# Kernel tuning notes

Measured on AMD Instinct MI355X. Metric: run time of the kernel, lower is better.

Reference implementation:

```python
import jax, jax.numpy as jnp
import numpy as np

N_NODES = 50000
N_EDGES = 1600000
IN_C, HID_C, OUT_C = 256, 256, 10


def setup_inputs() -> dict:
    key = jax.random.key(0)
    ks = jax.random.split(key, 8)
    x = jax.random.normal(ks[0], (N_NODES, IN_C), dtype=jnp.float32)
    edge_index = jax.random.randint(ks[1], (2, N_EDGES), 0, N_NODES, dtype=jnp.int64)
    s1 = 1.0 / np.sqrt(IN_C)
    s2 = 1.0 / np.sqrt(HID_C)
    W1l = jax.random.normal(ks[2], (IN_C, HID_C), dtype=jnp.float32) * s1
    W1r = jax.random.normal(ks[3], (IN_C, HID_C), dtype=jnp.float32) * s1
    b1 = jnp.zeros((HID_C,), dtype=jnp.float32)
    W2l = jax.random.normal(ks[4], (HID_C, OUT_C), dtype=jnp.float32) * s2
    W2r = jax.random.normal(ks[5], (HID_C, OUT_C), dtype=jnp.float32) * s2
    b2 = jnp.zeros((OUT_C,), dtype=jnp.float32)
    return {"x": x, "edge_index": edge_index, "W1l": W1l, "W1r": W1r,
            "b1": b1, "W2l": W2l, "W2r": W2r, "b2": b2}


def _mean_agg(x, src, dst, n):
    # scatter-mean of source features into destination nodes
    summed = jax.ops.segment_sum(x[src], dst, num_segments=n)  # [N, C]
    cnt = jax.ops.segment_sum(jnp.ones_like(dst, dtype=x.dtype), dst, num_segments=n)
    return summed / jnp.maximum(cnt, 1.0)[:, None]


def _sage_conv(x, src, dst, Wl, Wr, b):
    # PyG SAGEConv (mean aggr): lin_l(mean_j x_j) + lin_r(x_i) + bias
    n = x.shape[0]
    agg = _mean_agg(x, src, dst, n)
    return agg @ Wl + x @ Wr + b


def reference(x, edge_index, W1l, W1r, b1, W2l, W2r, b2):
    src = edge_index[0]
    dst = edge_index[1]
    h = _sage_conv(x, src, dst, W1l, W1r, b1)
    h = jax.nn.relu(h)  # dropout skipped: eval mode
    out = _sage_conv(h, src, dst, W2l, W2r, b2)
    return jax.nn.log_softmax(out, axis=1)
```

## Files before the change

### kernel.cpp

```cpp
#include <hip/hip_runtime.h>
#include <hip/hip_bf16.h>

#define N_NODES 50000
#define N_EDGES 1600000
#define IN_C 256
#define HID_C 256
#define OUT_C 10
#define CD_STRIDE 32
#define SLOT_CAP 96
#define NBUCKET 196
#define EBUF_CAP 9216

typedef short bf16x8 __attribute__((ext_vector_type(8)));
typedef float f32x4 __attribute__((ext_vector_type(4)));

static __device__ __forceinline__ float b2f(short v) {
    unsigned u = (unsigned)(unsigned short)v << 16;
    return __builtin_bit_cast(float, u);
}
static __device__ __forceinline__ short f2b(float f) {
    __hip_bfloat16 h = __float2bfloat16(f);
    return __builtin_bit_cast(short, h);
}

__global__ __launch_bounds__(256) void k_part(const int* __restrict__ src,
                                              const int* __restrict__ dst,
                                              int* __restrict__ g_cursor,
                                              int* __restrict__ ebuf) {
    __shared__ int hist[NBUCKET];
    __shared__ int base[NBUCKET];
    __shared__ int pos[NBUCKET];
    int tid = threadIdx.x;
    if (tid < NBUCKET) { hist[tid] = 0; pos[tid] = 0; }
    __syncthreads();

    int4 s[4], d[4];
    bool valid[4];
#pragma unroll
    for (int q = 0; q < 4; ++q) {
        int idx = blockIdx.x * 1024 + q * 256 + tid;
        valid[q] = (idx < N_EDGES / 4);
        if (valid[q]) {
            s[q] = ((const int4*)src)[idx];
            d[q] = ((const int4*)dst)[idx];
        }
    }
#pragma unroll
    for (int q = 0; q < 4; ++q) {
        if (valid[q]) {
            atomicAdd(&hist[d[q].x >> 8], 1);
            atomicAdd(&hist[d[q].y >> 8], 1);
            atomicAdd(&hist[d[q].z >> 8], 1);
            atomicAdd(&hist[d[q].w >> 8], 1);
        }
    }
    __syncthreads();
    if (tid < NBUCKET && hist[tid] > 0)
        base[tid] = atomicAdd(&g_cursor[tid], hist[tid]);
    __syncthreads();
#pragma unroll
    for (int q = 0; q < 4; ++q) {
        if (valid[q]) {
            int ss[4] = { s[q].x, s[q].y, s[q].z, s[q].w };
            int dd[4] = { d[q].x, d[q].y, d[q].z, d[q].w };
#pragma unroll
            for (int e = 0; e < 4; ++e) {
                int b = dd[e] >> 8;
                int p = base[b] + atomicAdd(&pos[b], 1);
                if (p < EBUF_CAP)
                    ebuf[b * EBUF_CAP + p] = ss[e] | ((dd[e] & 255) << 16);
            }
        }
    }
}

__global__ __launch_bounds__(256) void k_bucket(const int* __restrict__ ebuf,
                                                const int* __restrict__ g_cursor,
                                                int* __restrict__ cnt,
                                                unsigned short* __restrict__ slots) {
    __shared__ int lcnt[256];
    int b = blockIdx.x, tid = threadIdx.x;
    lcnt[tid] = 0;
    __syncthreads();
    int n_e = g_cursor[b];
    if (n_e > EBUF_CAP) n_e = EBUF_CAP;
    const int* eb = ebuf + b * EBUF_CAP;
    int n4 = n_e >> 2;
    for (int t = tid; t < n4; t += 256) {
        int4 v = ((const int4*)eb)[t];
        int vv[4] = { v.x, v.y, v.z, v.w };
#pragma unroll
        for (int e = 0; e < 4; ++e) {
            int dl = (vv[e] >> 16) & 255;
            int sv = vv[e] & 0xFFFF;
            int p = atomicAdd(&lcnt[dl], 1);
            if (p < SLOT_CAP) slots[(size_t)(b * 256 + dl) * SLOT_CAP + p] = (unsigned short)sv;
        }
    }
    for (int t = (n4 << 2) + tid; t < n_e; t += 256) {
        int vv = eb[t];
        int dl = (vv >> 16) & 255;
        int sv = vv & 0xFFFF;
        int p = atomicAdd(&lcnt[dl], 1);
        if (p < SLOT_CAP) slots[(size_t)(b * 256 + dl) * SLOT_CAP + p] = (unsigned short)sv;
    }
    __syncthreads();
    int nid = b * 256 + tid;
    if (nid < N_NODES) cnt[nid] = lcnt[tid];
}

__global__ void k_cvt_x(const float4* __restrict__ x, short4* __restrict__ xb) {
    int i = blockIdx.x * 256 + threadIdx.x;
    float4 v = x[i];
    short4 o = { f2b(v.x), f2b(v.y), f2b(v.z), f2b(v.w) };
    xb[i] = o;
}

__global__ void k_prep_w(const float* __restrict__ W1l, const float* __restrict__ W1r,
                         __hip_bfloat16* __restrict__ Wt) {
    int idx = blockIdx.x * 256 + threadIdx.x;
    int n = idx >> 8, k = idx & 255;
    float v = (n < HID_C) ? W1l[k * HID_C + n] : W1r[k * HID_C + (n - HID_C)];
    Wt[idx] = __float2bfloat16(v);
}

__global__ void k_prep_w2f(const float* __restrict__ W2l, const float* __restrict__ W2r,
                           float* __restrict__ Wt2f) {
    int idx = blockIdx.x * 256 + threadIdx.x;
    int r = idx >> 8, k = idx & 255;
    if (r < OUT_C) Wt2f[r * 256 + k] = W2l[k * OUT_C + r];
    else           Wt2f[(16 + r - OUT_C) * 256 + k] = W2r[k * OUT_C + (r - OUT_C)];
}

__global__ __launch_bounds__(256) void k_gemm1(
        const __hip_bfloat16* __restrict__ Xb, const __hip_bfloat16* __restrict__ Wt,
        const float* __restrict__ b1,
        __hip_bfloat16* __restrict__ Ab, __hip_bfloat16* __restrict__ Bh) {
    __shared__ short Smem[2 * 128 * 64];
    short* As = Smem;
    short* Bs = Smem + 128 * 64;
    int tid = threadIdx.x;
    int wave = tid >> 6, lane = tid & 63;
    int r = lane & 15, quad = lane >> 4;
    int wr = wave >> 1, wc = wave & 1;
    int m_base = blockIdx.x * 128;
    int n_base = blockIdx.y * 128;

    int srow = tid >> 3;
    int kb8  = (tid & 7) * 16;
    int swz  = kb8 ^ ((srow & 7) << 4);

    f32x4 acc[4][4];
#pragma unroll
    for (int i = 0; i < 4; ++i)
#pragma unroll
        for (int j = 0; j < 4; ++j) acc[i][j] = f32x4{0.f, 0.f, 0.f, 0.f};

    int4 av[4], bv[4];
#pragma unroll
    for (int q = 0; q < 4; ++q) {
        int grow = m_base + q * 32 + srow;
        if (grow > N_NODES - 1) grow = N_NODES - 1;
        av[q] = *(const int4*)((const char*)Xb + ((size_t)grow * 512 + kb8));
        int brow = n_base + q * 32 + srow;
        bv[q] = *(const int4*)((const char*)Wt + ((size_t)brow * 512 + kb8));
    }

    for (int kk = 0; kk < 4; ++kk) {
        if (kk) __syncthreads();
#pragma unroll
        for (int q = 0; q < 4; ++q) {
            *(int4*)((char*)As + (size_t)((q * 32 + srow) * 128 + swz)) = av[q];
            *(int4*)((char*)Bs + (size_t)((q * 32 + srow) * 128 + swz)) = bv[q];
        }
        __syncthreads();

        if (kk < 3) {
            int kbyte = (kk + 1) * 128 + kb8;
#pragma unroll
            for (int q = 0; q < 4; ++q) {
                int grow = m_base + q * 32 + srow;
                if (grow > N_NODES - 1) grow = N_NODES - 1;
                av[q] = *(const int4*)((const char*)Xb + ((size_t)grow * 512 + kbyte));
                int brow = n_base + q * 32 + srow;
                bv[q] = *(const int4*)((const char*)Wt + ((size_t)brow * 512 + kbyte));
            }
        }

#pragma unroll
        for (int s = 0; s < 2; ++s) {
            int kfb = (s * 64 + quad * 16) ^ ((r & 7) << 4);
            bf16x8 a[4], b[4];
#pragma unroll
            for (int i = 0; i < 4; ++i)
                a[i] = *(const bf16x8*)((const char*)As + (size_t)((wr * 64 + i * 16 + r) * 128) + kfb);
#pragma unroll
            for (int j = 0; j < 4; ++j)
                b[j] = *(const bf16x8*)((const char*)Bs + (size_t)((wc * 64 + j * 16 + r) * 128) + kfb);
#pragma unroll
            for (int i = 0; i < 4; ++i)
#pragma unroll
                for (int j = 0; j < 4; ++j)
                    acc[i][j] = __builtin_amdgcn_mfma_f32_16x16x32_bf16(a[i], b[j], acc[i][j], 0, 0, 0);
        }
    }

    __syncthreads();
    short* Cs = Smem;
    bool left = (n_base < HID_C);
#pragma unroll
    for (int j = 0; j < 4; ++j) {
        int coll = wc * 64 + 16 * j + r;
        float bias = left ? 0.f : b1[n_base + coll - HID_C];
#pragma unroll
        for (int i = 0; i < 4; ++i) {
#pragma unroll
            for (int ii = 0; ii < 4; ++ii) {
                int rowl = wr * 64 + 16 * i + quad * 4 + ii;
                int byteoff = (coll * 2) ^ ((rowl & 7) << 4);
                *(short*)((char*)Cs + rowl * 256 + byteoff) = f2b(acc[i][j][ii] + bias);
            }
        }
    }
    __syncthreads();

    int rrow = tid >> 4;
    int cchunk = (tid & 15) * 16;
    size_t colbyte = left ? (size_t)(n_base * 2) : (size_t)((n_base - HID_C) * 2);
    char* outp = left ? (char*)Ab : (char*)Bh;
    for (int rb = 0; rb < 128; rb += 16) {
        int rowl = rb + rrow;
        int4 v = *(const int4*)((const char*)Cs + rowl * 256 + (cchunk ^ ((rowl & 7) << 4)));
        int grow = m_base + rowl;
        if (grow < N_NODES)
            *(int4*)(outp + (size_t)grow * 512 + colbyte + cchunk) = v;
    }
}

__global__ __launch_bounds__(256) void k_agg1f(
        const __hip_bfloat16* __restrict__ Ab, const __hip_bfloat16* __restrict__ Bh,
        const int* __restrict__ cnt, const unsigned short* __restrict__ slots,
        const float* __restrict__ Wt2f, const float* __restrict__ b2,
        float* __restrict__ CD) {
    int wave = threadIdx.x >> 6, lane = threadIdx.x & 63;
    int nid = blockIdx.x * 4 + wave;
    int half = lane >> 5;
    int c8 = (lane & 31) * 8;
    const unsigned short* row = slots + (size_t)nid * SLOT_CAP;
    int n = cnt[nid];
    if (n > SLOT_CAP) n = SLOT_CAP;
    int mid = (n + 1) >> 1;
    int beg = half ? mid : 0;
    int end = half ? n : mid;

    float s0[8], s1[8], s2[8], s3[8];
#pragma unroll
    for (int j = 0; j < 8; ++j) { s0[j] = 0.f; s1[j] = 0.f; s2[j] = 0.f; s3[j] = 0.f; }

    const __hip_bfloat16* abc = Ab + c8;
    int e = beg;
    for (; e + 4 <= end; e += 4) {
        int i0 = row[e], i1 = row[e + 1], i2 = row[e + 2], i3 = row[e + 3];
        bf16x8 v0 = *(const bf16x8*)(abc + (size_t)i0 * HID_C);
        bf16x8 v1 = *(const bf16x8*)(abc + (size_t)i1 * HID_C);
        bf16x8 v2 = *(const bf16x8*)(abc + (size_t)i2 * HID_C);
        bf16x8 v3 = *(const bf16x8*)(abc + (size_t)i3 * HID_C);
#pragma unroll
        for (int j = 0; j < 8; ++j) {
            s0[j] += b2f(v0[j]); s1[j] += b2f(v1[j]);
            s2[j] += b2f(v2[j]); s3[j] += b2f(v3[j]);
        }
    }
    for (; e < end; ++e) {
        int i0 = row[e];
        bf16x8 v0 = *(const bf16x8*)(abc + (size_t)i0 * HID_C);
#pragma unroll
        for (int j = 0; j < 8; ++j) s0[j] += b2f(v0[j]);
    }
#pragma unroll
    for (int j = 0; j < 8; ++j) s0[j] += (s1[j] + s2[j]) + s3[j];
#pragma unroll
    for (int j = 0; j < 8; ++j) s0[j] += __shfl_down(s0[j], 32, 64);

    float h[8];
    float inv = 1.f / fmaxf((float)n, 1.f);
    if (half == 0) {
        bf16x8 bb = *(const bf16x8*)(Bh + (size_t)nid * HID_C + c8);
#pragma unroll
        for (int j = 0; j < 8; ++j)
            h[j] = fmaxf(s0[j] * inv + b2f(bb[j]), 0.f);
    }
#pragma unroll
    for (int j = 0; j < 8; ++j) h[j] = __shfl(h[j], lane & 31, 64);

    const float* wbase = Wt2f + (half ? 16 * 256 : 0);
    float acc[10];
#pragma unroll
    for (int j = 0; j < 10; ++j) {
        f32x4 w0 = *(const f32x4*)(wbase + j * 256 + c8);
        f32x4 w1 = *(const f32x4*)(wbase + j * 256 + c8 + 4);
        float a = h[0] * w0[0] + h[1] * w0[1] + h[2] * w0[2] + h[3] * w0[3]
                + h[4] * w1[0] + h[5] * w1[1] + h[6] * w1[2] + h[7] * w1[3];
#pragma unroll
        for (int off = 16; off > 0; off >>= 1)
            a += __shfl_down(a, off, 32);
        acc[j] = a;
    }
    if ((lane & 31) == 0) {
        float* o = CD + (size_t)nid * CD_STRIDE + half * 16;
        if (half == 0) {
#pragma unroll
            for (int j = 0; j < 10; ++j) o[j] = acc[j];
            o[10] = 0.f; o[11] = 0.f;
        } else {
#pragma unroll
            for (int j = 0; j < 10; ++j) o[j] = acc[j] + b2[j];
        }
    }
}

__global__ __launch_bounds__(256) void k_agg2(
        const float* __restrict__ CD, const int* __restrict__ cnt,
        const unsigned short* __restrict__ slots, float* __restrict__ out) {
    int wave = threadIdx.x >> 6, lane = threadIdx.x & 63;
    int half = lane >> 5, sub = lane & 31;
    int nid = blockIdx.x * 8 + wave * 2 + half;
    const unsigned short* row = slots + (size_t)nid * SLOT_CAP;
    int n = cnt[nid];
    if (n > SLOT_CAP) n = SLOT_CAP;
    float s[10];
#pragma unroll
    for (int j = 0; j < 10; ++j) s[j] = 0.f;
    for (int e = sub; e < n; e += 32) {
        const float* cr = CD + (size_t)row[e] * CD_STRIDE;
        f32x4 v0 = *(const f32x4*)cr;
        f32x4 v1 = *(const f32x4*)(cr + 4);
        f32x4 v2 = *(const f32x4*)(cr + 8);
#pragma unroll
        for (int j = 0; j < 4; ++j) { s[j] += v0[j]; s[4 + j] += v1[j]; }
        s[8] += v2[0]; s[9] += v2[1];
    }
#pragma unroll
    for (int j = 0; j < 10; ++j)
#pragma unroll
        for (int off = 16; off > 0; off >>= 1)
            s[j] += __shfl_down(s[j], off, 32);
    if (sub == 0) {
        float inv = 1.f / fmaxf((float)n, 1.f);
        float z[10], mx = -1e30f;
#pragma unroll
        for (int j = 0; j < 10; ++j) {
            z[j] = s[j] * inv + CD[(size_t)nid * CD_STRIDE + 16 + j];
            mx = fmaxf(mx, z[j]);
        }
        float se = 0.f;
#pragma unroll
        for (int j = 0; j < 10; ++j) se += expf(z[j] - mx);
        float lse = logf(se) + mx;
#pragma unroll
        for (int j = 0; j < 10; ++j) out[(size_t)nid * OUT_C + j] = z[j] - lse;
    }
}

extern "C" void kernel_launch(void* const* d_in, const int* in_sizes, int n_in,
                              void* d_out, int out_size, void* d_ws, size_t ws_size,
                              hipStream_t stream) {
    const float* x   = (const float*)d_in[0];
    const int*   ei  = (const int*)d_in[1];
    const float* W1l = (const float*)d_in[2];
    const float* W1r = (const float*)d_in[3];
    const float* b1  = (const float*)d_in[4];
    const float* W2l = (const float*)d_in[5];
    const float* W2r = (const float*)d_in[6];
    const float* b2  = (const float*)d_in[7];
    float* out = (float*)d_out;
    const int* src = ei;
    const int* dst = ei + N_EDGES;

    char* w = (char*)d_ws;
    size_t off = 0;
    auto alloc = [&](size_t bytes) -> void* {
        void* p = w + off;
        off = (off + bytes + 255) & ~(size_t)255;
        return p;
    };
    __hip_bfloat16* Xb   = (__hip_bfloat16*)alloc((size_t)N_NODES * IN_C * 2);
    __hip_bfloat16* Wt   = (__hip_bfloat16*)alloc((size_t)2 * HID_C * IN_C * 2);
    float*          Wt2f = (float*)alloc((size_t)32 * 256 * 4);
    __hip_bfloat16* Ab   = (__hip_bfloat16*)alloc((size_t)N_NODES * HID_C * 2);
    __hip_bfloat16* Bh   = (__hip_bfloat16*)alloc((size_t)N_NODES * HID_C * 2);
    float* CD = (float*)alloc((size_t)N_NODES * CD_STRIDE * 4);
    int* cnt      = (int*)alloc((size_t)N_NODES * 4);
    unsigned short* slots = (unsigned short*)alloc((size_t)N_NODES * SLOT_CAP * 2);
    int* g_cursor = (int*)alloc((size_t)NBUCKET * 4);
    int* ebuf     = (int*)alloc((size_t)NBUCKET * EBUF_CAP * 4);

    (void)hipMemsetAsync(g_cursor, 0, (size_t)NBUCKET * 4, stream);

    k_part<<<(N_EDGES / 4 + 1023) / 1024, 256, 0, stream>>>(src, dst, g_cursor, ebuf);
    k_bucket<<<NBUCKET, 256, 0, stream>>>(ebuf, g_cursor, cnt, slots);

    k_cvt_x<<<(N_NODES * IN_C / 4) / 256, 256, 0, stream>>>((const float4*)x, (short4*)Xb);
    k_prep_w<<<512, 256, 0, stream>>>(W1l, W1r, Wt);
    k_prep_w2f<<<20, 256, 0, stream>>>(W2l, W2r, Wt2f);

    k_gemm1<<<dim3((N_NODES + 127) / 128, 4), 256, 0, stream>>>(Xb, Wt, b1, Ab, Bh);
    k_agg1f<<<N_NODES / 4, 256, 0, stream>>>(Ab, Bh, cnt, slots, Wt2f, b2, CD);
    k_agg2<<<N_NODES / 8, 256, 0, stream>>>(CD, cnt, slots, out);
}
```

Measured before the change: 348.9 us.

## Fuse x bf16 conversion into GEMM, remap tiles per XCD, deepen gather unroll

Drops the separate fp32-to-bf16 conversion kernel for x: the first GEMM now reads fp32 rows directly and packs them to bf16 in registers. This removes one pass that wrote a bf16 copy and read it back. The GEMM grid is flattened and remapped so the four N-tiles of each M-tile land on the same XCD, which should improve L2 reuse of X. The aggregation gather loop is also unrolled to eight neighbours per iteration for more memory-level parallelism. In exchange, each GEMM tile now reads twice as many bytes of X, and the extra loads raise register pressure.

```diff
diff --git a/kernel.cpp b/kernel.cpp
--- a/kernel.cpp
+++ b/kernel.cpp
@@ -10,6 +10,7 @@
 #define SLOT_CAP 96
 #define NBUCKET 196
 #define EBUF_CAP 9216
+#define M_TILES 391
 
 typedef short bf16x8 __attribute__((ext_vector_type(8)));
 typedef float f32x4 __attribute__((ext_vector_type(4)));
@@ -21,6 +22,12 @@
 static __device__ __forceinline__ short f2b(float f) {
     __hip_bfloat16 h = __float2bfloat16(f);
     return __builtin_bit_cast(short, h);
+}
+static __device__ __forceinline__ int4 pack8(float4 a, float4 b) {
+    bf16x8 o;
+    o[0] = f2b(a.x); o[1] = f2b(a.y); o[2] = f2b(a.z); o[3] = f2b(a.w);
+    o[4] = f2b(b.x); o[5] = f2b(b.y); o[6] = f2b(b.z); o[7] = f2b(b.w);
+    return __builtin_bit_cast(int4, o);
 }
 
 __global__ __launch_bounds__(256) void k_part(const int* __restrict__ src,
@@ -109,13 +116,6 @@
     if (nid < N_NODES) cnt[nid] = lcnt[tid];
 }
 
-__global__ void k_cvt_x(const float4* __restrict__ x, short4* __restrict__ xb) {
-    int i = blockIdx.x * 256 + threadIdx.x;
-    float4 v = x[i];
-    short4 o = { f2b(v.x), f2b(v.y), f2b(v.z), f2b(v.w) };
-    xb[i] = o;
-}
-
 __global__ void k_prep_w(const float* __restrict__ W1l, const float* __restrict__ W1r,
                          __hip_bfloat16* __restrict__ Wt) {
     int idx = blockIdx.x * 256 + threadIdx.x;
@@ -133,21 +133,28 @@
 }
 
 __global__ __launch_bounds__(256) void k_gemm1(
-        const __hip_bfloat16* __restrict__ Xb, const __hip_bfloat16* __restrict__ Wt,
+        const float* __restrict__ X, const __hip_bfloat16* __restrict__ Wt,
         const float* __restrict__ b1,
         __hip_bfloat16* __restrict__ Ab, __hip_bfloat16* __restrict__ Bh) {
     __shared__ short Smem[2 * 128 * 64];
     short* As = Smem;
     short* Bs = Smem + 128 * 64;
+    int fid = blockIdx.x;
+    int xcd = fid & 7, slot = fid >> 3;
+    int m_t = (slot >> 2) * 8 + xcd;
+    if (m_t >= M_TILES) return;
+    int n_t = slot & 3;
+    int m_base = m_t * 128;
+    int n_base = n_t * 128;
+
     int tid = threadIdx.x;
     int wave = tid >> 6, lane = tid & 63;
     int r = lane & 15, quad = lane >> 4;
     int wr = wave >> 1, wc = wave & 1;
-    int m_base = blockIdx.x * 128;
-    int n_base = blockIdx.y * 128;
 
     int srow = tid >> 3;
     int kb8  = (tid & 7) * 16;
+    int kelem = (tid & 7) * 8;
     int swz  = kb8 ^ ((srow & 7) << 4);
 
     f32x4 acc[4][4];
@@ -161,7 +168,8 @@
     for (int q = 0; q < 4; ++q) {
         int grow = m_base + q * 32 + srow;
         if (grow > N_NODES - 1) grow = N_NODES - 1;
-        av[q] = *(const int4*)((const char*)Xb + ((size_t)grow * 512 + kb8));
+        const float* xp = X + (size_t)grow * IN_C + kelem;
+        av[q] = pack8(*(const float4*)xp, *(const float4*)(xp + 4));
         int brow = n_base + q * 32 + srow;
         bv[q] = *(const int4*)((const char*)Wt + ((size_t)brow * 512 + kb8));
     }
@@ -176,12 +184,14 @@
         __syncthreads();
 
         if (kk < 3) {
+            int ke = (kk + 1) * 64 + kelem;
             int kbyte = (kk + 1) * 128 + kb8;
 #pragma unroll
             for (int q = 0; q < 4; ++q) {
                 int grow = m_base + q * 32 + srow;
                 if (grow > N_NODES - 1) grow = N_NODES - 1;
-                av[q] = *(const int4*)((const char*)Xb + ((size_t)grow * 512 + kbyte));
+                const float* xp = X + (size_t)grow * IN_C + ke;
+                av[q] = pack8(*(const float4*)xp, *(const float4*)(xp + 4));
                 int brow = n_base + q * 32 + srow;
                 bv[q] = *(const int4*)((const char*)Wt + ((size_t)brow * 512 + kbyte));
             }
@@ -259,6 +269,25 @@
 
     const __hip_bfloat16* abc = Ab + c8;
     int e = beg;
+    for (; e + 8 <= end; e += 8) {
+        int i0 = row[e],     i1 = row[e + 1], i2 = row[e + 2], i3 = row[e + 3];
+        int i4 = row[e + 4], i5 = row[e + 5], i6 = row[e + 6], i7 = row[e + 7];
+        bf16x8 v0 = *(const bf16x8*)(abc + (size_t)i0 * HID_C);
+        bf16x8 v1 = *(const bf16x8*)(abc + (size_t)i1 * HID_C);
+        bf16x8 v2 = *(const bf16x8*)(abc + (size_t)i2 * HID_C);
+        bf16x8 v3 = *(const bf16x8*)(abc + (size_t)i3 * HID_C);
+        bf16x8 v4 = *(const bf16x8*)(abc + (size_t)i4 * HID_C);
+        bf16x8 v5 = *(const bf16x8*)(abc + (size_t)i5 * HID_C);
+        bf16x8 v6 = *(const bf16x8*)(abc + (size_t)i6 * HID_C);
+        bf16x8 v7 = *(const bf16x8*)(abc + (size_t)i7 * HID_C);
+#pragma unroll
+        for (int j = 0; j < 8; ++j) {
+            s0[j] += b2f(v0[j]) + b2f(v4[j]);
+            s1[j] += b2f(v1[j]) + b2f(v5[j]);
+            s2[j] += b2f(v2[j]) + b2f(v6[j]);
+            s3[j] += b2f(v3[j]) + b2f(v7[j]);
+        }
+    }
     for (; e + 4 <= end; e += 4) {
         int i0 = row[e], i1 = row[e + 1], i2 = row[e + 2], i3 = row[e + 3];
         bf16x8 v0 = *(const bf16x8*)(abc + (size_t)i0 * HID_C);
@@ -384,7 +413,6 @@
         off = (off + bytes + 255) & ~(size_t)255;
         return p;
     };
-    __hip_bfloat16* Xb   = (__hip_bfloat16*)alloc((size_t)N_NODES * IN_C * 2);
     __hip_bfloat16* Wt   = (__hip_bfloat16*)alloc((size_t)2 * HID_C * IN_C * 2);
     float*          Wt2f = (float*)alloc((size_t)32 * 256 * 4);
     __hip_bfloat16* Ab   = (__hip_bfloat16*)alloc((size_t)N_NODES * HID_C * 2);
@@ -400,11 +428,10 @@
     k_part<<<(N_EDGES / 4 + 1023) / 1024, 256, 0, stream>>>(src, dst, g_cursor, ebuf);
     k_bucket<<<NBUCKET, 256, 0, stream>>>(ebuf, g_cursor, cnt, slots);
 
-    k_cvt_x<<<(N_NODES * IN_C / 4) / 256, 256, 0, stream>>>((const float4*)x, (short4*)Xb);
     k_prep_w<<<512, 256, 0, stream>>>(W1l, W1r, Wt);
     k_prep_w2f<<<20, 256, 0, stream>>>(W2l, W2r, Wt2f);
 
-    k_gemm1<<<dim3((N_NODES + 127) / 128, 4), 256, 0, stream>>>(Xb, Wt, b1, Ab, Bh);
+    k_gemm1<<<8 * 196, 256, 0, stream>>>(x, Wt, b1, Ab, Bh);
     k_agg1f<<<N_NODES / 4, 256, 0, stream>>>(Ab, Bh, cnt, slots, Wt2f, b2, CD);
     k_agg2<<<N_NODES / 8, 256, 0, stream>>>(CD, cnt, slots, out);
 }
```

New measurement: 327.0 us. 6.3% less time.
